# Performance work log

Measured on AMD Instinct MI355X. Metric: run time of the kernel, lower is better.

The kernel has to match this reference:

```python
import jax, jax.numpy as jnp
import numpy as np

N_NODES = 50000
N_EDGES = 800000
IN_CH = 512
HID = 512


def setup_inputs() -> dict:
    key = jax.random.key(0)
    ks = jax.random.split(key, 8)
    x = jax.random.normal(ks[0], (N_NODES, IN_CH), dtype=jnp.float32)
    edge_index = jax.random.randint(ks[1], (2, N_EDGES), 0, N_NODES, dtype=jnp.int64)
    s_in = 1.0 / np.sqrt(IN_CH)
    s_h = 1.0 / np.sqrt(HID)
    W1 = jax.random.uniform(ks[2], (IN_CH, HID), jnp.float32, -s_in, s_in)
    b1 = jnp.zeros((HID,), jnp.float32)
    W2 = jax.random.uniform(ks[3], (HID, HID), jnp.float32, -s_h, s_h)
    b2 = jnp.zeros((HID,), jnp.float32)
    Wo = jax.random.uniform(ks[4], (HID, 1), jnp.float32, -s_h, s_h)
    bo = jnp.zeros((1,), jnp.float32)
    return {"x": x, "edge_index": edge_index, "W1": W1, "b1": b1,
            "W2": W2, "b2": b2, "Wo": Wo, "bo": bo}


def _gcn_norm(edge_index, n):
    # add self-loops, compute symmetric normalization deg^{-1/2} per edge
    loop = jnp.arange(n, dtype=edge_index.dtype)
    src = jnp.concatenate([edge_index[0], loop])  # [E+N]
    dst = jnp.concatenate([edge_index[1], loop])
    deg = jax.ops.segment_sum(jnp.ones_like(dst, dtype=jnp.float32), dst,
                              num_segments=n)
    dinv = jnp.where(deg > 0, jax.lax.rsqrt(jnp.maximum(deg, 1.0)), 0.0)
    norm = dinv[src] * dinv[dst]  # [E+N]
    return src, dst, norm


def _gcn_conv(h, src, dst, norm, W, b, n):
    h = h @ W                          # [N, H] dense GEMM first (PyG order)
    msg = h[src] * norm[:, None]       # gather + per-edge scale
    out = jax.ops.segment_sum(msg, dst, num_segments=n)  # scatter-add
    return out + b


def reference(x, edge_index, W1, b1, W2, b2, Wo, bo):
    n = x.shape[0]
    src, dst, norm = _gcn_norm(edge_index, n)
    h = jax.nn.relu(_gcn_conv(x, src, dst, norm, W1, b1, n))
    h = jax.nn.relu(_gcn_conv(h, src, dst, norm, W2, b2, n))
    logits = (h @ Wo + bo)[:, 0]       # [N]
    return jax.nn.softmax(logits, axis=0)
```

## Files before the change

kernel.cpp:

```cpp
#include <hip/hip_runtime.h>

#define NN 50000
#define NP 50176
#define NE 800000
#define CH 512
#define NB 196
#define PB_TRANS 2048
#define PB_DEG 782
#define PB_PERM 6
#define SMB 49
#define GB1 (4 * (NP / 128))
#define BKB ((NE / 2 + 255) / 256)

typedef __bf16 bf16x8 __attribute__((ext_vector_type(8)));
typedef float f32x4 __attribute__((ext_vector_type(4)));
typedef float f32x2 __attribute__((ext_vector_type(2)));
typedef unsigned short u16x8 __attribute__((ext_vector_type(8)));

static __device__ __forceinline__ unsigned short f2b(float f){
  unsigned u = __builtin_bit_cast(unsigned, f);
  u = (u + 0x7fffu + ((u >> 16) & 1u)) >> 16;
  return (unsigned short)u;
}
static __device__ __forceinline__ float b2f(unsigned short h){
  unsigned u = ((unsigned)h) << 16;
  return __builtin_bit_cast(float, u);
}
static __device__ __forceinline__ float rdlane_f(float v, int l){
  return __builtin_bit_cast(float, __builtin_amdgcn_readlane(__builtin_bit_cast(int, v), l));
}
static __device__ __forceinline__ unsigned pack2(float f0, float f1){
  unsigned u0 = __builtin_bit_cast(unsigned, f0) + 0x8000u;
  unsigned u1 = __builtin_bit_cast(unsigned, f1) + 0x8000u;
  return __builtin_amdgcn_perm(u1, u0, 0x07060302u);
}
static __device__ __forceinline__ int lam(int p){
  return (p & ~63) | (((p & 3) << 4) + ((p & 63) >> 2));
}

__global__ void k_prep(const float* __restrict__ W1, const float* __restrict__ W2,
                       unsigned short* __restrict__ W1t, unsigned short* __restrict__ W2t,
                       const int* __restrict__ ei, int* __restrict__ deg,
                       int* __restrict__ rank,
                       const float* __restrict__ b1, const float* __restrict__ b2,
                       const float* __restrict__ Wo, float* __restrict__ b1p,
                       float* __restrict__ b2p, float* __restrict__ Wop){
  const int b = blockIdx.x, t = threadIdx.x;
  if (b < PB_TRANS){
    int idx = (b & 1023) * 256 + t;
    int n = idx >> 9, p = idx & (CH - 1);
    if (b < 1024)
      W1t[n * CH + p] = f2b(W1[p * CH + n]);
    else
      W2t[n * CH + p] = f2b(W2[lam(p) * CH + n]);
  } else if (b < PB_TRANS + PB_DEG){
    int e4 = ((b - PB_TRANS) * 256 + t) * 4;
    if (e4 < NE){
      int4 d = *(const int4*)(ei + NE + e4);
      int4 r;
      r.x = atomicAdd(&deg[d.x], 1);
      r.y = atomicAdd(&deg[d.y], 1);
      r.z = atomicAdd(&deg[d.z], 1);
      r.w = atomicAdd(&deg[d.w], 1);
      *(int4*)(rank + e4) = r;
    }
  } else {
    int idx = (b - PB_TRANS - PB_DEG) * 256 + t;
    int which = idx >> 9, p = idx & (CH - 1);
    int l = lam(p);
    if (which == 0) b1p[p] = b1[l];
    else if (which == 1) b2p[p] = b2[l];
    else Wop[p] = Wo[l];
  }
}

__global__ void k_blocksum(const int* __restrict__ deg, int* __restrict__ bsum){
  __shared__ int sh[4];
  const int t = threadIdx.x;
  int i = blockIdx.x * 256 + t;
  int v = (i < NN) ? deg[i] : 0;
  #pragma unroll
  for (int off = 32; off > 0; off >>= 1) v += __shfl_down(v, off, 64);
  if ((t & 63) == 0) sh[t >> 6] = v;
  __syncthreads();
  if (t == 0) bsum[blockIdx.x] = sh[0] + sh[1] + sh[2] + sh[3];
}

__global__ void k_scanoff(const int* __restrict__ bsum, int* __restrict__ boff,
                          int* __restrict__ row_ptr){
  __shared__ int sh[256];
  const int t = threadIdx.x;
  int v = (t < NB) ? bsum[t] : 0;
  sh[t] = v; __syncthreads();
  for (int d = 1; d < 256; d <<= 1){
    int add = (t >= d) ? sh[t - d] : 0;
    __syncthreads();
    sh[t] += add;
    __syncthreads();
  }
  if (t < NB) boff[t] = sh[t] - v;
  if (t == 255) row_ptr[NN] = sh[255];
}

__global__ void k_scatter(const int* __restrict__ deg, const int* __restrict__ boff,
                          int* __restrict__ row_ptr, float* __restrict__ dinv){
  __shared__ int sh[256];
  const int t = threadIdx.x;
  int i = blockIdx.x * 256 + t;
  int d = (i < NN) ? deg[i] : 0;
  sh[t] = d; __syncthreads();
  for (int dd = 1; dd < 256; dd <<= 1){
    int add = (t >= dd) ? sh[t - dd] : 0;
    __syncthreads();
    sh[t] += add;
    __syncthreads();
  }
  if (i < NN){
    row_ptr[i] = sh[t] - d + boff[blockIdx.x];
    dinv[i] = rsqrtf((float)d + 1.0f);
  }
}

template<bool CVT>
static __device__ __forceinline__ void gemm_body(
    const int bx, const int t,
    const void* __restrict__ Av, const unsigned short* __restrict__ Bt,
    unsigned char* __restrict__ C,
    unsigned short (&As)[2][4096], unsigned short (&Bs)[2][4096]){
  const int wave = t >> 6, lane = t & 63;
  const int quad = lane >> 4, l15 = lane & 15;
  const int mw = (wave & 1) * 64;
  const int nw = (wave >> 1) * 64;
  const int g = bx >> 5, rem = bx & 31;
  const int rt = g * 8 + (rem & 7);
  const int rowBase = rt * 128;
  const int nBase = (rem >> 3) * 128;

  const int lr = lane >> 2;
  const int lc = (lane & 3) * 8;
  const int lr8 = lane >> 3;
  const int lc8 = lane & 7;
  const unsigned short* Bg0 = Bt + (size_t)(nBase + wave * 32 + lr) * CH + lc;
  const int boff = wave * 1024;
  const float* X = (const float*)Av;
  const unsigned short* Ag0 = (const unsigned short*)Av;
  if (!CVT) Ag0 += (size_t)(rowBase + wave * 32 + lr) * CH + lc;
  const int aoff = wave * 1024;

  int arow[4]; size_t asrc[4];
  if (CVT){
    #pragma unroll
    for (int q=0;q<4;q++){
      arow[q] = wave * 32 + q * 8 + lr8;
      int gr = rowBase + arow[q];
      if (gr >= NN) gr = 0;
      asrc[q] = (size_t)gr * CH + lc8 * 4;
    }
  }

  f32x4 acc[4][4];
  #pragma unroll
  for (int i=0;i<4;i++)
    #pragma unroll
    for (int j=0;j<4;j++) acc[i][j] = 0;

  float4 apre[4];
  if (CVT){
    #pragma unroll
    for (int q=0;q<4;q++) apre[q] = *(const float4*)(X + asrc[q]);
    #pragma unroll
    for (int q=0;q<4;q++){
      uint2 pk; pk.x = pack2(apre[q].x, apre[q].y); pk.y = pack2(apre[q].z, apre[q].w);
      *(uint2*)&As[0][arow[q] * 32 + lc8 * 4] = pk;
    }
  } else {
    #pragma unroll
    for (int q=0;q<2;q++)
      __builtin_amdgcn_global_load_lds(
        (const __attribute__((address_space(1))) void*)(Ag0 + (size_t)q*16*CH),
        (__attribute__((address_space(3))) void*)(&As[0][aoff + q*512]), 16, 0, 0);
  }
  #pragma unroll
  for (int q=0;q<2;q++)
    __builtin_amdgcn_global_load_lds(
      (const __attribute__((address_space(1))) void*)(Bg0 + (size_t)q*16*CH),
      (__attribute__((address_space(3))) void*)(&Bs[0][boff + q*512]), 16, 0, 0);

  for (int it = 0; it < 16; it++){
    const int cur = it & 1, nxt = cur ^ 1;
    __syncthreads();
    if (it < 15){
      const int kb = (it + 1) * 32;
      if (CVT){
        #pragma unroll
        for (int q=0;q<4;q++) apre[q] = *(const float4*)(X + asrc[q] + kb);
      } else {
        #pragma unroll
        for (int q=0;q<2;q++)
          __builtin_amdgcn_global_load_lds(
            (const __attribute__((address_space(1))) void*)(Ag0 + (size_t)q*16*CH + kb),
            (__attribute__((address_space(3))) void*)(&As[nxt][aoff + q*512]), 16, 0, 0);
      }
      #pragma unroll
      for (int q=0;q<2;q++)
        __builtin_amdgcn_global_load_lds(
          (const __attribute__((address_space(1))) void*)(Bg0 + (size_t)q*16*CH + kb),
          (__attribute__((address_space(3))) void*)(&Bs[nxt][boff + q*512]), 16, 0, 0);
    }
    bf16x8 af[4], bfr[4];
    #pragma unroll
    for (int i=0;i<4;i++)
      af[i] = __builtin_bit_cast(bf16x8,
              *(const u16x8*)&As[cur][(mw + i*16 + l15) * 32 + quad * 8]);
    #pragma unroll
    for (int j=0;j<4;j++)
      bfr[j] = __builtin_bit_cast(bf16x8,
              *(const u16x8*)&Bs[cur][(nw + j*16 + l15) * 32 + quad * 8]);
    #pragma unroll
    for (int i=0;i<4;i++)
      #pragma unroll
      for (int j=0;j<4;j++)
        acc[i][j] = __builtin_amdgcn_mfma_f32_16x16x32_bf16(af[i], bfr[j], acc[i][j], 0, 0, 0);
    if (CVT && it < 15){
      #pragma unroll
      for (int q=0;q<4;q++){
        uint2 pk; pk.x = pack2(apre[q].x, apre[q].y); pk.y = pack2(apre[q].z, apre[q].w);
        *(uint2*)&As[nxt][arow[q] * 32 + lc8 * 4] = pk;
      }
    }
  }

  #pragma unroll
  for (int i=0;i<4;i++){
    #pragma unroll
    for (int r=0;r<4;r++){
      int row = rowBase + mw + i*16 + quad*4 + r;
      int w0 = 0;
      w0 = __builtin_amdgcn_cvt_pk_fp8_f32(acc[i][0][r], acc[i][1][r], w0, false);
      w0 = __builtin_amdgcn_cvt_pk_fp8_f32(acc[i][2][r], acc[i][3][r], w0, true);
      *(unsigned*)(C + (size_t)row * CH + nBase + nw + l15*4) = (unsigned)w0;
    }
  }
}

__launch_bounds__(256, 4)
__global__ void k_gemm1(const float* __restrict__ x, const unsigned short* __restrict__ W1t,
                        unsigned char* __restrict__ C){
  __shared__ __align__(16) unsigned short As[2][4096];
  __shared__ __align__(16) unsigned short Bs[2][4096];
  gemm_body<true>(blockIdx.x, threadIdx.x, x, W1t, C, As, Bs);
}

__global__ void k_bucket(const int* __restrict__ ei, const int* __restrict__ row_ptr,
                         const int* __restrict__ rank, int* __restrict__ csr_src){
  int e2 = (blockIdx.x * 256 + threadIdx.x) * 2;
  if (e2 < NE){
    int2 src = *(const int2*)(ei + e2);
    int2 dst = *(const int2*)(ei + NE + e2);
    int2 rk  = *(const int2*)(rank + e2);
    csr_src[row_ptr[dst.x] + rk.x] = src.x;
    csr_src[row_ptr[dst.y] + rk.y] = src.y;
  }
}

__launch_bounds__(256, 4)
__global__ void k_gemm2(const unsigned short* __restrict__ A,
                        const unsigned short* __restrict__ Bt,
                        unsigned char* __restrict__ C){
  __shared__ __align__(16) unsigned short As[2][4096];
  __shared__ __align__(16) unsigned short Bs[2][4096];
  gemm_body<false>(blockIdx.x, threadIdx.x, A, Bt, C, As, Bs);
}

template<bool HEAD>
__launch_bounds__(256)
__global__ void k_agg(const unsigned char* __restrict__ h, const int* __restrict__ row_ptr,
                      const int* __restrict__ csr_src, const float* __restrict__ dinv,
                      const float* __restrict__ bias, unsigned short* __restrict__ out,
                      const float* __restrict__ Wo, const float* __restrict__ bo,
                      float* __restrict__ logits){
  const int node = blockIdx.x * 4 + (threadIdx.x >> 6);
  const int lane = threadIdx.x & 63;
  float acc[8];
  #pragma unroll
  for (int k=0;k<8;k++) acc[k] = 0.f;
  const int rp = row_ptr[node], re = row_ptr[node + 1];
  for (int base = rp; base < re; base += 64){
    int cnt = re - base; if (cnt > 64) cnt = 64;
    int s = 0; float w = 0.f;
    if (base + lane < re){ s = csr_src[base + lane]; w = dinv[s]; }
    int j = 0;
    for (; j + 8 <= cnt; j += 8){
      int ss[8]; float ww[8]; uint2 hv[8];
      #pragma unroll
      for (int u=0;u<8;u++){
        ss[u] = __builtin_amdgcn_readlane(s, j + u);
        ww[u] = rdlane_f(w, j + u);
      }
      #pragma unroll
      for (int u=0;u<8;u++)
        hv[u] = *(const uint2*)(h + (size_t)ss[u] * CH + lane * 8);
      #pragma unroll
      for (int u=0;u<8;u++){
        f32x2 p0 = __builtin_amdgcn_cvt_pk_f32_fp8((int)hv[u].x, false);
        f32x2 p1 = __builtin_amdgcn_cvt_pk_f32_fp8((int)hv[u].x, true);
        f32x2 p2 = __builtin_amdgcn_cvt_pk_f32_fp8((int)hv[u].y, false);
        f32x2 p3 = __builtin_amdgcn_cvt_pk_f32_fp8((int)hv[u].y, true);
        acc[0] += ww[u] * p0.x; acc[1] += ww[u] * p0.y;
        acc[2] += ww[u] * p1.x; acc[3] += ww[u] * p1.y;
        acc[4] += ww[u] * p2.x; acc[5] += ww[u] * p2.y;
        acc[6] += ww[u] * p3.x; acc[7] += ww[u] * p3.y;
      }
    }
    for (; j < cnt; j++){
      int ss = __builtin_amdgcn_readlane(s, j);
      float ww = rdlane_f(w, j);
      uint2 hv = *(const uint2*)(h + (size_t)ss * CH + lane * 8);
      f32x2 p0 = __builtin_amdgcn_cvt_pk_f32_fp8((int)hv.x, false);
      f32x2 p1 = __builtin_amdgcn_cvt_pk_f32_fp8((int)hv.x, true);
      f32x2 p2 = __builtin_amdgcn_cvt_pk_f32_fp8((int)hv.y, false);
      f32x2 p3 = __builtin_amdgcn_cvt_pk_f32_fp8((int)hv.y, true);
      acc[0] += ww * p0.x; acc[1] += ww * p0.y;
      acc[2] += ww * p1.x; acc[3] += ww * p1.y;
      acc[4] += ww * p2.x; acc[5] += ww * p2.y;
      acc[6] += ww * p3.x; acc[7] += ww * p3.y;
    }
  }
  const float di = dinv[node];
  uint2 hsv = *(const uint2*)(h + (size_t)node * CH + lane * 8);
  f32x2 s0 = __builtin_amdgcn_cvt_pk_f32_fp8((int)hsv.x, false);
  f32x2 s1 = __builtin_amdgcn_cvt_pk_f32_fp8((int)hsv.x, true);
  f32x2 s2 = __builtin_amdgcn_cvt_pk_f32_fp8((int)hsv.y, false);
  f32x2 s3 = __builtin_amdgcn_cvt_pk_f32_fp8((int)hsv.y, true);
  float hsf[8] = {s0.x, s0.y, s1.x, s1.y, s2.x, s2.y, s3.x, s3.y};
  const float4* bp = (const float4*)(bias + lane * 8);
  float4 bv0 = bp[0], bv1 = bp[1];
  float bb[8] = {bv0.x,bv0.y,bv0.z,bv0.w,bv1.x,bv1.y,bv1.z,bv1.w};
  if (HEAD){
    const float4* wp = (const float4*)(Wo + lane * 8);
    float4 w0 = wp[0], w1 = wp[1];
    float wv[8] = {w0.x,w0.y,w0.z,w0.w,w1.x,w1.y,w1.z,w1.w};
    float v = 0.f;
    #pragma unroll
    for (int k=0;k<8;k++){
      float r = fmaxf(di * acc[k] + di * di * hsf[k] + bb[k], 0.f);
      v += r * wv[k];
    }
    #pragma unroll
    for (int off = 32; off > 0; off >>= 1) v += __shfl_down(v, off, 64);
    if (lane == 0) logits[node] = v + bo[0];
  } else {
    u16x8 o;
    #pragma unroll
    for (int k=0;k<8;k++){
      float r = fmaxf(di * acc[k] + di * di * hsf[k] + bb[k], 0.f);
      o[k] = f2b(r);
    }
    *(u16x8*)(out + (size_t)node * CH + lane * 8) = o;
  }
}

__global__ void k_smpart(const float* __restrict__ logits, float* __restrict__ pm,
                         float* __restrict__ ps){
  __shared__ float shm[16], shs[16];
  const int t = threadIdx.x;
  const int i = blockIdx.x * 1024 + t;
  float v = (i < NN) ? logits[i] : -3.4e38f;
  float m = v;
  #pragma unroll
  for (int off = 32; off > 0; off >>= 1) m = fmaxf(m, __shfl_down(m, off, 64));
  if ((t & 63) == 0) shm[t >> 6] = m;
  __syncthreads();
  if (t < 64){
    float mm = (t < 16) ? shm[t] : -3.4e38f;
    #pragma unroll
    for (int off = 8; off > 0; off >>= 1) mm = fmaxf(mm, __shfl_down(mm, off, 64));
    if (t == 0) shm[0] = mm;
  }
  __syncthreads();
  const float bm = shm[0];
  float s = (i < NN) ? expf(v - bm) : 0.f;
  #pragma unroll
  for (int off = 32; off > 0; off >>= 1) s += __shfl_down(s, off, 64);
  if ((t & 63) == 0) shs[t >> 6] = s;
  __syncthreads();
  if (t < 64){
    float sss = (t < 16) ? shs[t] : 0.f;
    #pragma unroll
    for (int off = 8; off > 0; off >>= 1) sss += __shfl_down(sss, off, 64);
    if (t == 0){ pm[blockIdx.x] = bm; ps[blockIdx.x] = sss; }
  }
}

__global__ void k_smwrite(const float* __restrict__ logits, const float* __restrict__ pm,
                          const float* __restrict__ ps, float* __restrict__ out){
  __shared__ float shMS[2];
  const int t = threadIdx.x;
  if (t < 64){
    float m = (t < SMB) ? pm[t] : -3.4e38f;
    float M = m;
    #pragma unroll
    for (int off = 32; off > 0; off >>= 1) M = fmaxf(M, __shfl_down(M, off, 64));
    M = rdlane_f(M, 0);
    float s = (t < SMB) ? ps[t] * expf(m - M) : 0.f;
    #pragma unroll
    for (int off = 32; off > 0; off >>= 1) s += __shfl_down(s, off, 64);
    if (t == 0){ shMS[0] = M; shMS[1] = s; }
  }
  __syncthreads();
  int i = blockIdx.x * blockDim.x + t;
  if (i < NN) out[i] = expf(logits[i] - shMS[0]) / shMS[1];
}

extern "C" void kernel_launch(void* const* d_in, const int* in_sizes, int n_in,
                              void* d_out, int out_size, void* d_ws, size_t ws_size,
                              hipStream_t stream){
  const float* x  = (const float*)d_in[0];
  const int*   ei = (const int*)d_in[1];
  const float* W1 = (const float*)d_in[2];
  const float* b1 = (const float*)d_in[3];
  const float* W2 = (const float*)d_in[4];
  const float* b2 = (const float*)d_in[5];
  const float* Wo = (const float*)d_in[6];
  const float* bo = (const float*)d_in[7];
  float* out = (float*)d_out;

  char* ws = (char*)d_ws;
  size_t off = 0;
  auto alloc = [&](size_t bytes) -> void* {
    void* p = ws + off;
    off = (off + bytes + 255) & ~(size_t)255;
    return p;
  };
  unsigned short* B0  = (unsigned short*)alloc((size_t)NP * CH * 2);
  unsigned char*  B1  = (unsigned char*)alloc((size_t)NP * CH);
  unsigned short* W1t = (unsigned short*)alloc((size_t)CH * CH * 2);
  unsigned short* W2t = (unsigned short*)alloc((size_t)CH * CH * 2);
  int*   deg     = (int*)alloc((size_t)NN * 4);
  float* dinv    = (float*)alloc((size_t)NN * 4);
  int*   row_ptr = (int*)alloc((size_t)(NN + 1) * 4);
  int*   rank    = (int*)alloc((size_t)NE * 4);
  int*   csr     = (int*)alloc((size_t)NE * 4);
  float* logits  = (float*)alloc((size_t)NN * 4);
  int*   bsum    = (int*)alloc((size_t)NB * 4);
  int*   boff    = (int*)alloc((size_t)NB * 4);
  float* pm      = (float*)alloc((size_t)SMB * 4);
  float* ps      = (float*)alloc((size_t)SMB * 4);
  float* b1p     = (float*)alloc((size_t)CH * 4);
  float* b2p     = (float*)alloc((size_t)CH * 4);
  float* Wop     = (float*)alloc((size_t)CH * 4);

  hipMemsetAsync(deg, 0, (size_t)NN * 4, stream);
  k_prep<<<PB_TRANS + PB_DEG + PB_PERM, 256, 0, stream>>>(
      W1, W2, W1t, W2t, ei, deg, rank, b1, b2, Wo, b1p, b2p, Wop);
  k_blocksum<<<NB, 256, 0, stream>>>(deg, bsum);
  k_scanoff<<<1, 256, 0, stream>>>(bsum, boff, row_ptr);
  k_scatter<<<NB, 256, 0, stream>>>(deg, boff, row_ptr, dinv);

  k_bucket<<<BKB, 256, 0, stream>>>(ei, row_ptr, rank, csr);
  k_gemm1<<<GB1, 256, 0, stream>>>(x, W1t, B1);
  k_agg<false><<<NN / 4, 256, 0, stream>>>(B1, row_ptr, csr, dinv, b1p, B0,
                                           Wop, bo, logits);
  k_gemm2<<<GB1, 256, 0, stream>>>(B0, W2t, B1);
  k_agg<true><<<NN / 4, 256, 0, stream>>>(B1, row_ptr, csr, dinv, b2p, B0,
                                          Wop, bo, logits);

  k_smpart<<<SMB, 1024, 0, stream>>>(logits, pm, ps);
  k_smwrite<<<NB, 256, 0, stream>>>(logits, pm, ps, out);
}
```

Before: 435.3 us.

## Triple-buffer GEMM LDS tiles with explicit vmcnt waits and single barrier

Both GEMM kernels move from double to triple-buffered LDS staging, prefetching two K-tiles ahead. Explicit s_waitcnt with partial vmcnt counts and a raw s_barrier replace the full __syncthreads, so loads for tile it+2 can stay in flight while tile it is computed. LDS use per block grows to 48KB and launch bounds drop from 4 to 3 blocks per CU. The hand-set vmcnt counts depend on how many memory instructions the compiler emits per tile, so correctness relies on that staying fixed.

Result: slower. 455.7 us (+4.7%).

```diff
diff --git a/kernel.cpp b/kernel.cpp
--- a/kernel.cpp
+++ b/kernel.cpp
@@ -126,7 +126,7 @@
     const int bx, const int t,
     const void* __restrict__ Av, const unsigned short* __restrict__ Bt,
     unsigned char* __restrict__ C,
-    unsigned short (&As)[2][4096], unsigned short (&Bs)[2][4096]){
+    unsigned short (&As)[3][4096], unsigned short (&Bs)[3][4096]){
   const int wave = t >> 6, lane = t & 63;
   const int quad = lane >> 4, l15 = lane & 15;
   const int mw = (wave & 1) * 64;
@@ -164,33 +164,64 @@
     #pragma unroll
     for (int j=0;j<4;j++) acc[i][j] = 0;
 
-  float4 apre[4];
   if (CVT){
-    #pragma unroll
-    for (int q=0;q<4;q++) apre[q] = *(const float4*)(X + asrc[q]);
-    #pragma unroll
-    for (int q=0;q<4;q++){
-      uint2 pk; pk.x = pack2(apre[q].x, apre[q].y); pk.y = pack2(apre[q].z, apre[q].w);
-      *(uint2*)&As[0][arow[q] * 32 + lc8 * 4] = pk;
-    }
-  } else {
+    float4 a0[4], a1[4];
+    #pragma unroll
+    for (int q=0;q<4;q++) a0[q] = *(const float4*)(X + asrc[q]);
     #pragma unroll
     for (int q=0;q<2;q++)
       __builtin_amdgcn_global_load_lds(
-        (const __attribute__((address_space(1))) void*)(Ag0 + (size_t)q*16*CH),
-        (__attribute__((address_space(3))) void*)(&As[0][aoff + q*512]), 16, 0, 0);
-  }
-  #pragma unroll
-  for (int q=0;q<2;q++)
-    __builtin_amdgcn_global_load_lds(
-      (const __attribute__((address_space(1))) void*)(Bg0 + (size_t)q*16*CH),
-      (__attribute__((address_space(3))) void*)(&Bs[0][boff + q*512]), 16, 0, 0);
-
+        (const __attribute__((address_space(1))) void*)(Bg0 + (size_t)q*16*CH),
+        (__attribute__((address_space(3))) void*)(&Bs[0][boff + q*512]), 16, 0, 0);
+    #pragma unroll
+    for (int q=0;q<4;q++) a1[q] = *(const float4*)(X + asrc[q] + 32);
+    #pragma unroll
+    for (int q=0;q<2;q++)
+      __builtin_amdgcn_global_load_lds(
+        (const __attribute__((address_space(1))) void*)(Bg0 + (size_t)q*16*CH + 32),
+        (__attribute__((address_space(3))) void*)(&Bs[1][boff + q*512]), 16, 0, 0);
+    #pragma unroll
+    for (int q=0;q<4;q++){
+      uint2 pk; pk.x = pack2(a0[q].x, a0[q].y); pk.y = pack2(a0[q].z, a0[q].w);
+      *(uint2*)&As[0][arow[q] * 32 + lc8 * 4] = pk;
+    }
+    #pragma unroll
+    for (int q=0;q<4;q++){
+      uint2 pk; pk.x = pack2(a1[q].x, a1[q].y); pk.y = pack2(a1[q].z, a1[q].w);
+      *(uint2*)&As[1][arow[q] * 32 + lc8 * 4] = pk;
+    }
+  } else {
+    #pragma unroll
+    for (int tt=0;tt<2;tt++){
+      #pragma unroll
+      for (int q=0;q<2;q++)
+        __builtin_amdgcn_global_load_lds(
+          (const __attribute__((address_space(1))) void*)(Ag0 + (size_t)q*16*CH + tt*32),
+          (__attribute__((address_space(3))) void*)(&As[tt][aoff + q*512]), 16, 0, 0);
+      #pragma unroll
+      for (int q=0;q<2;q++)
+        __builtin_amdgcn_global_load_lds(
+          (const __attribute__((address_space(1))) void*)(Bg0 + (size_t)q*16*CH + tt*32),
+          (__attribute__((address_space(3))) void*)(&Bs[tt][boff + q*512]), 16, 0, 0);
+    }
+  }
+
+  int cur = 0;
+  float4 apre[4];
   for (int it = 0; it < 16; it++){
-    const int cur = it & 1, nxt = cur ^ 1;
-    __syncthreads();
+    const int b2 = cur ? cur - 1 : 2;
     if (it < 15){
-      const int kb = (it + 1) * 32;
+      if (CVT) asm volatile("s_waitcnt vmcnt(2) lgkmcnt(0)" ::: "memory");
+      else     asm volatile("s_waitcnt vmcnt(4) lgkmcnt(0)" ::: "memory");
+    } else {
+      asm volatile("s_waitcnt vmcnt(0) lgkmcnt(0)" ::: "memory");
+    }
+    __builtin_amdgcn_sched_barrier(0);
+    __builtin_amdgcn_s_barrier();
+    __builtin_amdgcn_sched_barrier(0);
+
+    if (it < 14){
+      const int kb = (it + 2) * 32;
       if (CVT){
         #pragma unroll
         for (int q=0;q<4;q++) apre[q] = *(const float4*)(X + asrc[q] + kb);
@@ -199,14 +230,15 @@
         for (int q=0;q<2;q++)
           __builtin_amdgcn_global_load_lds(
             (const __attribute__((address_space(1))) void*)(Ag0 + (size_t)q*16*CH + kb),
-            (__attribute__((address_space(3))) void*)(&As[nxt][aoff + q*512]), 16, 0, 0);
+            (__attribute__((address_space(3))) void*)(&As[b2][aoff + q*512]), 16, 0, 0);
       }
       #pragma unroll
       for (int q=0;q<2;q++)
         __builtin_amdgcn_global_load_lds(
           (const __attribute__((address_space(1))) void*)(Bg0 + (size_t)q*16*CH + kb),
-          (__attribute__((address_space(3))) void*)(&Bs[nxt][boff + q*512]), 16, 0, 0);
-    }
+          (__attribute__((address_space(3))) void*)(&Bs[b2][boff + q*512]), 16, 0, 0);
+    }
+
     bf16x8 af[4], bfr[4];
     #pragma unroll
     for (int i=0;i<4;i++)
@@ -221,13 +253,15 @@
       #pragma unroll
       for (int j=0;j<4;j++)
         acc[i][j] = __builtin_amdgcn_mfma_f32_16x16x32_bf16(af[i], bfr[j], acc[i][j], 0, 0, 0);
-    if (CVT && it < 15){
+
+    if (CVT && it < 14){
       #pragma unroll
       for (int q=0;q<4;q++){
         uint2 pk; pk.x = pack2(apre[q].x, apre[q].y); pk.y = pack2(apre[q].z, apre[q].w);
-        *(uint2*)&As[nxt][arow[q] * 32 + lc8 * 4] = pk;
+        *(uint2*)&As[b2][arow[q] * 32 + lc8 * 4] = pk;
       }
     }
+    cur = (cur == 2) ? 0 : cur + 1;
   }
 
   #pragma unroll
@@ -243,11 +277,11 @@
   }
 }
 
-__launch_bounds__(256, 4)
+__launch_bounds__(256, 3)
 __global__ void k_gemm1(const float* __restrict__ x, const unsigned short* __restrict__ W1t,
                         unsigned char* __restrict__ C){
-  __shared__ __align__(16) unsigned short As[2][4096];
-  __shared__ __align__(16) unsigned short Bs[2][4096];
+  __shared__ __align__(16) unsigned short As[3][4096];
+  __shared__ __align__(16) unsigned short Bs[3][4096];
   gemm_body<true>(blockIdx.x, threadIdx.x, x, W1t, C, As, Bs);
 }
 
@@ -263,12 +297,12 @@
   }
 }
 
-__launch_bounds__(256, 4)
+__launch_bounds__(256, 3)
 __global__ void k_gemm2(const unsigned short* __restrict__ A,
                         const unsigned short* __restrict__ Bt,
                         unsigned char* __restrict__ C){
-  __shared__ __align__(16) unsigned short As[2][4096];
-  __shared__ __align__(16) unsigned short Bs[2][4096];
+  __shared__ __align__(16) unsigned short As[3][4096];
+  __shared__ __align__(16) unsigned short Bs[3][4096];
   gemm_body<false>(blockIdx.x, threadIdx.x, A, Bt, C, As, Bs);
 }
 
```

## Double GEMM K-tile to 64 and XOR-swizzle LDS layout

Applied to the files above, without the earlier changes.

The GEMM main loop now stages 64 K-elements per iteration, split into two 32-wide sub-tiles, so it runs 8 iterations instead of 16. That halves the number of barriers and load-issue phases. The LDS tile column offset is also XOR-swizzled by row bits on both the writes and the fragment reads, to reduce bank conflicts. Shared memory per block doubles and the launch-bounds occupancy hint drops from 4 to 2, so latency hiding may suffer.

Result: no change. 431.5 us (-0.9%).

```diff
diff --git a/kernel.cpp b/kernel.cpp
--- a/kernel.cpp
+++ b/kernel.cpp
@@ -126,7 +126,7 @@
     const int bx, const int t,
     const void* __restrict__ Av, const unsigned short* __restrict__ Bt,
     unsigned char* __restrict__ C,
-    unsigned short (&As)[2][4096], unsigned short (&Bs)[2][4096]){
+    unsigned short (&As)[2][8192], unsigned short (&Bs)[2][8192]){
   const int wave = t >> 6, lane = t & 63;
   const int quad = lane >> 4, l15 = lane & 15;
   const int mw = (wave & 1) * 64;
@@ -137,17 +137,18 @@
   const int nBase = (rem >> 3) * 128;
 
   const int lr = lane >> 2;
-  const int lc = (lane & 3) * 8;
+  const int lcs = (((lane & 3) ^ ((lr >> 1) & 3)) * 8);
   const int lr8 = lane >> 3;
   const int lc8 = lane & 7;
-  const unsigned short* Bg0 = Bt + (size_t)(nBase + wave * 32 + lr) * CH + lc;
+  const unsigned short* Bg0 = Bt + (size_t)(nBase + wave * 32 + lr) * CH + lcs;
   const int boff = wave * 1024;
   const float* X = (const float*)Av;
   const unsigned short* Ag0 = (const unsigned short*)Av;
-  if (!CVT) Ag0 += (size_t)(rowBase + wave * 32 + lr) * CH + lc;
+  if (!CVT) Ag0 += (size_t)(rowBase + wave * 32 + lr) * CH + lcs;
   const int aoff = wave * 1024;
 
   int arow[4]; size_t asrc[4];
+  int wswz = 0;
   if (CVT){
     #pragma unroll
     for (int q=0;q<4;q++){
@@ -156,7 +157,9 @@
       if (gr >= NN) gr = 0;
       asrc[q] = (size_t)gr * CH + lc8 * 4;
     }
-  }
+    wswz = (lc8 * 4) ^ ((lr8 & 6) << 2);
+  }
+  const int rsw = (l15 & 6) << 2;
 
   f32x4 acc[4][4];
   #pragma unroll
@@ -164,69 +167,93 @@
     #pragma unroll
     for (int j=0;j<4;j++) acc[i][j] = 0;
 
-  float4 apre[4];
+  float4 apre[2][4];
+
   if (CVT){
     #pragma unroll
-    for (int q=0;q<4;q++) apre[q] = *(const float4*)(X + asrc[q]);
-    #pragma unroll
-    for (int q=0;q<4;q++){
-      uint2 pk; pk.x = pack2(apre[q].x, apre[q].y); pk.y = pack2(apre[q].z, apre[q].w);
-      *(uint2*)&As[0][arow[q] * 32 + lc8 * 4] = pk;
-    }
+    for (int p=0;p<2;p++)
+      #pragma unroll
+      for (int q=0;q<4;q++) apre[p][q] = *(const float4*)(X + asrc[q] + p*32);
+    #pragma unroll
+    for (int p=0;p<2;p++)
+      #pragma unroll
+      for (int q=0;q<4;q++){
+        uint2 pk; pk.x = pack2(apre[p][q].x, apre[p][q].y);
+        pk.y = pack2(apre[p][q].z, apre[p][q].w);
+        *(uint2*)&As[0][p*4096 + arow[q]*32 + wswz] = pk;
+      }
   } else {
     #pragma unroll
-    for (int q=0;q<2;q++)
+    for (int p=0;p<2;p++)
+      #pragma unroll
+      for (int gg=0;gg<2;gg++)
+        __builtin_amdgcn_global_load_lds(
+          (const __attribute__((address_space(1))) void*)(Ag0 + (size_t)gg*16*CH + p*32),
+          (__attribute__((address_space(3))) void*)(&As[0][p*4096 + aoff + gg*512]), 16, 0, 0);
+  }
+  #pragma unroll
+  for (int p=0;p<2;p++)
+    #pragma unroll
+    for (int gg=0;gg<2;gg++)
       __builtin_amdgcn_global_load_lds(
-        (const __attribute__((address_space(1))) void*)(Ag0 + (size_t)q*16*CH),
-        (__attribute__((address_space(3))) void*)(&As[0][aoff + q*512]), 16, 0, 0);
-  }
-  #pragma unroll
-  for (int q=0;q<2;q++)
-    __builtin_amdgcn_global_load_lds(
-      (const __attribute__((address_space(1))) void*)(Bg0 + (size_t)q*16*CH),
-      (__attribute__((address_space(3))) void*)(&Bs[0][boff + q*512]), 16, 0, 0);
-
-  for (int it = 0; it < 16; it++){
+        (const __attribute__((address_space(1))) void*)(Bg0 + (size_t)gg*16*CH + p*32),
+        (__attribute__((address_space(3))) void*)(&Bs[0][p*4096 + boff + gg*512]), 16, 0, 0);
+
+  for (int it = 0; it < 8; it++){
     const int cur = it & 1, nxt = cur ^ 1;
     __syncthreads();
-    if (it < 15){
-      const int kb = (it + 1) * 32;
+    if (it < 7){
+      const int kb = (it + 1) * 64;
       if (CVT){
         #pragma unroll
-        for (int q=0;q<4;q++) apre[q] = *(const float4*)(X + asrc[q] + kb);
+        for (int p=0;p<2;p++)
+          #pragma unroll
+          for (int q=0;q<4;q++) apre[p][q] = *(const float4*)(X + asrc[q] + kb + p*32);
       } else {
         #pragma unroll
-        for (int q=0;q<2;q++)
+        for (int p=0;p<2;p++)
+          #pragma unroll
+          for (int gg=0;gg<2;gg++)
+            __builtin_amdgcn_global_load_lds(
+              (const __attribute__((address_space(1))) void*)(Ag0 + (size_t)gg*16*CH + kb + p*32),
+              (__attribute__((address_space(3))) void*)(&As[nxt][p*4096 + aoff + gg*512]), 16, 0, 0);
+      }
+      #pragma unroll
+      for (int p=0;p<2;p++)
+        #pragma unroll
+        for (int gg=0;gg<2;gg++)
           __builtin_amdgcn_global_load_lds(
-            (const __attribute__((address_space(1))) void*)(Ag0 + (size_t)q*16*CH + kb),
-            (__attribute__((address_space(3))) void*)(&As[nxt][aoff + q*512]), 16, 0, 0);
-      }
-      #pragma unroll
-      for (int q=0;q<2;q++)
-        __builtin_amdgcn_global_load_lds(
-          (const __attribute__((address_space(1))) void*)(Bg0 + (size_t)q*16*CH + kb),
-          (__attribute__((address_space(3))) void*)(&Bs[nxt][boff + q*512]), 16, 0, 0);
-    }
-    bf16x8 af[4], bfr[4];
-    #pragma unroll
-    for (int i=0;i<4;i++)
-      af[i] = __builtin_bit_cast(bf16x8,
-              *(const u16x8*)&As[cur][(mw + i*16 + l15) * 32 + quad * 8]);
-    #pragma unroll
-    for (int j=0;j<4;j++)
-      bfr[j] = __builtin_bit_cast(bf16x8,
-              *(const u16x8*)&Bs[cur][(nw + j*16 + l15) * 32 + quad * 8]);
-    #pragma unroll
-    for (int i=0;i<4;i++)
+            (const __attribute__((address_space(1))) void*)(Bg0 + (size_t)gg*16*CH + kb + p*32),
+            (__attribute__((address_space(3))) void*)(&Bs[nxt][p*4096 + boff + gg*512]), 16, 0, 0);
+    }
+
+    #pragma unroll
+    for (int ks=0;ks<2;ks++){
+      bf16x8 af[4], bfr[4];
+      #pragma unroll
+      for (int i=0;i<4;i++)
+        af[i] = __builtin_bit_cast(bf16x8,
+                *(const u16x8*)&As[cur][ks*4096 + (mw + i*16 + l15)*32 + (quad*8 ^ rsw)]);
       #pragma unroll
       for (int j=0;j<4;j++)
-        acc[i][j] = __builtin_amdgcn_mfma_f32_16x16x32_bf16(af[i], bfr[j], acc[i][j], 0, 0, 0);
-    if (CVT && it < 15){
-      #pragma unroll
-      for (int q=0;q<4;q++){
-        uint2 pk; pk.x = pack2(apre[q].x, apre[q].y); pk.y = pack2(apre[q].z, apre[q].w);
-        *(uint2*)&As[nxt][arow[q] * 32 + lc8 * 4] = pk;
-      }
+        bfr[j] = __builtin_bit_cast(bf16x8,
+                *(const u16x8*)&Bs[cur][ks*4096 + (nw + j*16 + l15)*32 + (quad*8 ^ rsw)]);
+      #pragma unroll
+      for (int i=0;i<4;i++)
+        #pragma unroll
+        for (int j=0;j<4;j++)
+          acc[i][j] = __builtin_amdgcn_mfma_f32_16x16x32_bf16(af[i], bfr[j], acc[i][j], 0, 0, 0);
+    }
+
+    if (CVT && it < 7){
+      #pragma unroll
+      for (int p=0;p<2;p++)
+        #pragma unroll
+        for (int q=0;q<4;q++){
+          uint2 pk; pk.x = pack2(apre[p][q].x, apre[p][q].y);
+          pk.y = pack2(apre[p][q].z, apre[p][q].w);
+          *(uint2*)&As[nxt][p*4096 + arow[q]*32 + wswz] = pk;
+        }
     }
   }
 
@@ -243,11 +270,11 @@
   }
 }
 
-__launch_bounds__(256, 4)
+__launch_bounds__(256, 2)
 __global__ void k_gemm1(const float* __restrict__ x, const unsigned short* __restrict__ W1t,
                         unsigned char* __restrict__ C){
-  __shared__ __align__(16) unsigned short As[2][4096];
-  __shared__ __align__(16) unsigned short Bs[2][4096];
+  __shared__ __align__(16) unsigned short As[2][8192];
+  __shared__ __align__(16) unsigned short Bs[2][8192];
   gemm_body<true>(blockIdx.x, threadIdx.x, x, W1t, C, As, Bs);
 }
 
@@ -263,12 +290,12 @@
   }
 }
 
-__launch_bounds__(256, 4)
+__launch_bounds__(256, 2)
 __global__ void k_gemm2(const unsigned short* __restrict__ A,
                         const unsigned short* __restrict__ Bt,
                         unsigned char* __restrict__ C){
-  __shared__ __align__(16) unsigned short As[2][4096];
-  __shared__ __align__(16) unsigned short Bs[2][4096];
+  __shared__ __align__(16) unsigned short As[2][8192];
+  __shared__ __align__(16) unsigned short Bs[2][8192];
   gemm_body<false>(blockIdx.x, threadIdx.x, A, Bt, C, As, Bs);
 }
 
```
